# Performance work log

Measured on AMD Instinct MI355X. Metric: run time of the kernel, lower is better.

The kernel has to match this reference:

```python
import jax, jax.numpy as jnp
import numpy as np

LEAK_RATE = 0.9
SPECTRAL_RADIUS = 0.95
DENSITY = 0.1
RES_SCALE = 1.0
IN_SCALE = 0.1
H = 1024   # reservoir_size
CH = 4     # channel_size
D = 64     # input_size
B = 16
T = 1024


def setup_inputs() -> dict:
    key = jax.random.key(0)
    kx, kw, ki, km = jax.random.split(key, 4)
    x = jax.random.normal(kx, (B, CH, T, D), dtype=jnp.float32)
    # reservoir weights: uniform(-scale, scale), sparsified by density mask,
    # then rescaled so largest singular value == spectral_radius
    W = np.asarray(jax.random.uniform(kw, (H, H), minval=-RES_SCALE, maxval=RES_SCALE))
    mask = np.asarray(jax.random.uniform(km, (H, H)) < DENSITY, dtype=np.float32)
    W = W * mask
    rho = float(np.linalg.svd(W, compute_uv=False).max())
    if rho > 0:
        W = W * (SPECTRAL_RADIUS / rho)
    W_res = jnp.asarray(W, dtype=jnp.float32)
    W_in = jax.random.uniform(ki, (H, D * CH), minval=-IN_SCALE, maxval=IN_SCALE, dtype=jnp.float32)
    return {"x": x, "W_in": W_in, "W_res": W_res}


def reference(x, W_in, W_res):
    Bsz, ch, Tlen, Din = x.shape
    # u_t = x[:,:,t,:].reshape(B, ch*D); precompute all input projections at once
    u = jnp.transpose(x, (2, 0, 1, 3)).reshape(Tlen, Bsz, ch * Din)   # [T, B, ch*D]
    inp = jnp.einsum('tbf,hf->tbh', u, W_in)                           # [T, B, H]

    def step(state, inp_t):
        # state: [B, ch, H]; inp_t: [B, H] broadcast over channels (unsqueeze(1))
        state_update = jnp.einsum('bch,hk->bck', state, W_res)
        new_state = LEAK_RATE * jnp.tanh(inp_t[:, None, :] + state_update) \
                    + (1.0 - LEAK_RATE) * state
        return new_state, new_state

    init = jnp.zeros((Bsz, ch, W_res.shape[0]), dtype=x.dtype)
    _, states = jax.lax.scan(step, init, inp)          # [T, B, ch, H]
    return jnp.transpose(states, (1, 2, 0, 3))          # [B, ch, T, H]
```

## Files before the change

kernel.cpp:

```cpp
#include <hip/hip_runtime.h>
#include <stdint.h>


#define H_  1024
#define T_  1024
#define B_  16
#define CH_ 4
#define D_  64
#define F_  256

__global__ __launch_bounds__(256) void inp_gemm(const float* __restrict__ x,
                                                const float* __restrict__ W_in,
                                                float* __restrict__ out)
{
    __shared__ float U[64 * 68];
    __shared__ float Wt[64 * 66];
    const int k0 = blockIdx.x * 64;
    const int t0 = blockIdx.y * 64;
    const int b  = blockIdx.z;
    const int tid = threadIdx.x;
    const int ty = tid >> 4, tx = tid & 15;

    float4 acc[4];
    acc[0] = float4{0.f,0.f,0.f,0.f}; acc[1] = acc[0]; acc[2] = acc[0]; acc[3] = acc[0];

    for (int fc = 0; fc < 4; ++fc) {
        {
            const int t_l = tid >> 2, fs = tid & 3;
            const float* src = x + ((size_t)(b * CH_ + fc) * T_ + (t0 + t_l)) * D_ + fs * 16;
            float* dst = &U[t_l * 68 + fs * 16];
            #pragma unroll
            for (int q = 0; q < 4; ++q)
                ((float4*)dst)[q] = ((const float4*)src)[q];
        }
        {
            const int k_l = tid >> 2, fs = tid & 3;
            const float* src = W_in + (size_t)(k0 + k_l) * F_ + fc * 64 + fs * 16;
            float4 v[4];
            #pragma unroll
            for (int q = 0; q < 4; ++q) v[q] = ((const float4*)src)[q];
            #pragma unroll
            for (int q = 0; q < 4; ++q) {
                Wt[(fs*16 + q*4 + 0) * 66 + k_l] = v[q].x;
                Wt[(fs*16 + q*4 + 1) * 66 + k_l] = v[q].y;
                Wt[(fs*16 + q*4 + 2) * 66 + k_l] = v[q].z;
                Wt[(fs*16 + q*4 + 3) * 66 + k_l] = v[q].w;
            }
        }
        __syncthreads();
        #pragma unroll 4
        for (int f4 = 0; f4 < 16; ++f4) {
            float4 a[4], bk[4];
            #pragma unroll
            for (int r = 0; r < 4; ++r)  a[r]  = *(const float4*)&U[(ty*4 + r) * 68 + f4*4];
            #pragma unroll
            for (int kk = 0; kk < 4; ++kk) bk[kk] = *(const float4*)&Wt[(f4*4 + kk) * 66 + tx*4];
            #pragma unroll
            for (int r = 0; r < 4; ++r) {
                const float4 av = a[r];
                acc[r].x = fmaf(av.x, bk[0].x, acc[r].x); acc[r].y = fmaf(av.x, bk[0].y, acc[r].y);
                acc[r].z = fmaf(av.x, bk[0].z, acc[r].z); acc[r].w = fmaf(av.x, bk[0].w, acc[r].w);
                acc[r].x = fmaf(av.y, bk[1].x, acc[r].x); acc[r].y = fmaf(av.y, bk[1].y, acc[r].y);
                acc[r].z = fmaf(av.y, bk[1].z, acc[r].z); acc[r].w = fmaf(av.y, bk[1].w, acc[r].w);
                acc[r].x = fmaf(av.z, bk[2].x, acc[r].x); acc[r].y = fmaf(av.z, bk[2].y, acc[r].y);
                acc[r].z = fmaf(av.z, bk[2].z, acc[r].z); acc[r].w = fmaf(av.z, bk[2].w, acc[r].w);
                acc[r].x = fmaf(av.w, bk[3].x, acc[r].x); acc[r].y = fmaf(av.w, bk[3].y, acc[r].y);
                acc[r].z = fmaf(av.w, bk[3].z, acc[r].z); acc[r].w = fmaf(av.w, bk[3].w, acc[r].w);
            }
        }
        __syncthreads();
    }
    #pragma unroll
    for (int r = 0; r < 4; ++r) {
        float* dst = out + ((size_t)(b * CH_) * T_ + (t0 + ty*4 + r)) * H_ + k0 + tx*4;
        *(float4*)dst = acc[r];
    }
}

#define LOAD32_SC0(v, a0, a1)                                                     \
    asm volatile(                                                                 \
        "global_load_dwordx2 %0, %32, off sc0\n\t"                                \
        "global_load_dwordx2 %1, %32, off offset:256 sc0\n\t"                     \
        "global_load_dwordx2 %2, %32, off offset:512 sc0\n\t"                     \
        "global_load_dwordx2 %3, %32, off offset:768 sc0\n\t"                     \
        "global_load_dwordx2 %4, %32, off offset:1024 sc0\n\t"                    \
        "global_load_dwordx2 %5, %32, off offset:1280 sc0\n\t"                    \
        "global_load_dwordx2 %6, %32, off offset:1536 sc0\n\t"                    \
        "global_load_dwordx2 %7, %32, off offset:1792 sc0\n\t"                    \
        "global_load_dwordx2 %8, %32, off offset:2048 sc0\n\t"                    \
        "global_load_dwordx2 %9, %32, off offset:2304 sc0\n\t"                    \
        "global_load_dwordx2 %10, %32, off offset:2560 sc0\n\t"                   \
        "global_load_dwordx2 %11, %32, off offset:2816 sc0\n\t"                   \
        "global_load_dwordx2 %12, %32, off offset:3072 sc0\n\t"                   \
        "global_load_dwordx2 %13, %32, off offset:3328 sc0\n\t"                   \
        "global_load_dwordx2 %14, %32, off offset:3584 sc0\n\t"                   \
        "global_load_dwordx2 %15, %32, off offset:3840 sc0\n\t"                   \
        "global_load_dwordx2 %16, %33, off sc0\n\t"                               \
        "global_load_dwordx2 %17, %33, off offset:256 sc0\n\t"                    \
        "global_load_dwordx2 %18, %33, off offset:512 sc0\n\t"                    \
        "global_load_dwordx2 %19, %33, off offset:768 sc0\n\t"                    \
        "global_load_dwordx2 %20, %33, off offset:1024 sc0\n\t"                   \
        "global_load_dwordx2 %21, %33, off offset:1280 sc0\n\t"                   \
        "global_load_dwordx2 %22, %33, off offset:1536 sc0\n\t"                   \
        "global_load_dwordx2 %23, %33, off offset:1792 sc0\n\t"                   \
        "global_load_dwordx2 %24, %33, off offset:2048 sc0\n\t"                   \
        "global_load_dwordx2 %25, %33, off offset:2304 sc0\n\t"                   \
        "global_load_dwordx2 %26, %33, off offset:2560 sc0\n\t"                   \
        "global_load_dwordx2 %27, %33, off offset:2816 sc0\n\t"                   \
        "global_load_dwordx2 %28, %33, off offset:3072 sc0\n\t"                   \
        "global_load_dwordx2 %29, %33, off offset:3328 sc0\n\t"                   \
        "global_load_dwordx2 %30, %33, off offset:3584 sc0\n\t"                   \
        "global_load_dwordx2 %31, %33, off offset:3840 sc0\n\t"                   \
        "s_waitcnt vmcnt(0)"                                                      \
        : "=&v"(v[0]),  "=&v"(v[1]),  "=&v"(v[2]),  "=&v"(v[3]),                  \
          "=&v"(v[4]),  "=&v"(v[5]),  "=&v"(v[6]),  "=&v"(v[7]),                  \
          "=&v"(v[8]),  "=&v"(v[9]),  "=&v"(v[10]), "=&v"(v[11]),                 \
          "=&v"(v[12]), "=&v"(v[13]), "=&v"(v[14]), "=&v"(v[15]),                 \
          "=&v"(v[16]), "=&v"(v[17]), "=&v"(v[18]), "=&v"(v[19]),                 \
          "=&v"(v[20]), "=&v"(v[21]), "=&v"(v[22]), "=&v"(v[23]),                 \
          "=&v"(v[24]), "=&v"(v[25]), "=&v"(v[26]), "=&v"(v[27]),                 \
          "=&v"(v[28]), "=&v"(v[29]), "=&v"(v[30]), "=&v"(v[31])                  \
        : "v"(a0), "v"(a1)                                                        \
        : "memory")

__global__ __launch_bounds__(256, 1) void esn_recur(const float* __restrict__ Wres,
                                                    float* __restrict__ out,
                                                    unsigned long long* __restrict__ hbuf)
{
    __shared__ float smem[17664];
    const int bx  = blockIdx.x;
    const int grp = bx & 7;
    const int j   = bx >> 3;
    const int C0  = j * 32;
    const int tid = threadIdx.x;
    const int kr  = tid >> 3;
    const int cg  = tid & 7;
    const int es   = tid >> 5;
    const int ecol = tid & 31;
    const int bc   = grp * 8 + es;
    const size_t seqBase = (size_t)bc * (T_ * H_);
    const size_t inpBase = (size_t)(bc & ~3) * (T_ * H_);

    float4 w4[32];
    #pragma unroll
    for (int kk = 0; kk < 32; ++kk)
        w4[kk] = *(const float4*)&Wres[(size_t)(kr * 32 + kk) * H_ + C0 + cg * 4];

    for (int idx = tid; idx < 17664; idx += 256) smem[idx] = 0.f;
    __syncthreads();

    int use_fast = 1;
    unsigned long long  pend_pv   = 0;
    unsigned long long* pend_addr = nullptr;

    for (int t = 0; t < T_; ++t) {
        float inp_v;
        if (t > 0) {
            unsigned long long v[32];
            const unsigned long long* src =
                hbuf + ((size_t)(((t - 1) & 1) * 64 + bc)) * H_ + ecol;
            const unsigned long long a0 = (unsigned long long)src;
            const unsigned long long a1 = a0 + 4096;
            const unsigned int want = (unsigned int)t;
            unsigned int bad = 1u;
            if (use_fast) {
                int spins = 0;
                for (;;) {
                    LOAD32_SC0(v, a0, a1);
                    bad = 0u;
                    #pragma unroll
                    for (int q = 0; q < 32; ++q)
                        bad |= ((unsigned int)(v[q] >> 32)) ^ want;
                    if (!bad) break;
                    if (++spins >= 64) break;
                    __builtin_amdgcn_s_sleep(1);
                }
                if (bad) use_fast = 0;
            }
            if (bad) {
                int guard = 0;
                for (;;) {
                    #pragma unroll
                    for (int q = 0; q < 32; ++q)
                        v[q] = __hip_atomic_load(src + q * 32,
                                                 __ATOMIC_RELAXED, __HIP_MEMORY_SCOPE_AGENT);
                    unsigned int b2 = 0u;
                    #pragma unroll
                    for (int q = 0; q < 32; ++q)
                        b2 |= ((unsigned int)(v[q] >> 32)) ^ want;
                    if (!b2 || ++guard > (1 << 16)) break;
                    __builtin_amdgcn_s_sleep(2);
                }
            }
            inp_v = out[inpBase + (size_t)t * H_ + C0 + ecol];
            float* dst = &smem[es * 1152 + ecol];
            #pragma unroll
            for (int q = 0; q < 32; ++q)
                dst[q * 36] = __uint_as_float((unsigned int)(v[q] & 0xffffffffu));
        } else {
            inp_v = out[inpBase + C0 + ecol];
        }
        __syncthreads();

        if (t > 0)
            __hip_atomic_store(pend_addr, pend_pv,
                               __ATOMIC_RELAXED, __HIP_MEMORY_SCOPE_AGENT);

        float4 acc4[8];
        #pragma unroll
        for (int s = 0; s < 8; ++s) acc4[s] = float4{0.f,0.f,0.f,0.f};
        const int hbase = kr * 36;
        #pragma unroll
        for (int c8 = 0; c8 < 8; ++c8) {
            const float4 wv0 = w4[c8*4+0], wv1 = w4[c8*4+1], wv2 = w4[c8*4+2], wv3 = w4[c8*4+3];
            #pragma unroll
            for (int s = 0; s < 8; ++s) {
                const float4 hv = *(const float4*)&smem[s * 1152 + hbase + c8 * 4];
                float4 a = acc4[s];
                a.x = fmaf(hv.x, wv0.x, a.x); a.y = fmaf(hv.x, wv0.y, a.y);
                a.z = fmaf(hv.x, wv0.z, a.z); a.w = fmaf(hv.x, wv0.w, a.w);
                a.x = fmaf(hv.y, wv1.x, a.x); a.y = fmaf(hv.y, wv1.y, a.y);
                a.z = fmaf(hv.y, wv1.z, a.z); a.w = fmaf(hv.y, wv1.w, a.w);
                a.x = fmaf(hv.z, wv2.x, a.x); a.y = fmaf(hv.z, wv2.y, a.y);
                a.z = fmaf(hv.z, wv2.z, a.z); a.w = fmaf(hv.z, wv2.w, a.w);
                a.x = fmaf(hv.w, wv3.x, a.x); a.y = fmaf(hv.w, wv3.y, a.y);
                a.z = fmaf(hv.w, wv3.z, a.z); a.w = fmaf(hv.w, wv3.w, a.w);
                acc4[s] = a;
            }
        }
        #pragma unroll
        for (int s = 0; s < 8; ++s) {
            float* pp = &smem[9216 + s * 1056 + kr * 33 + cg * 4];
            pp[0] = acc4[s].x; pp[1] = acc4[s].y; pp[2] = acc4[s].z; pp[3] = acc4[s].w;
        }
        __syncthreads();

        float s0 = 0.f, s1 = 0.f, s2 = 0.f, s3 = 0.f;
        #pragma unroll
        for (int k2 = 0; k2 < 32; k2 += 4) {
            s0 += smem[9216 + es * 1056 + (k2+0) * 33 + ecol];
            s1 += smem[9216 + es * 1056 + (k2+1) * 33 + ecol];
            s2 += smem[9216 + es * 1056 + (k2+2) * 33 + ecol];
            s3 += smem[9216 + es * 1056 + (k2+3) * 33 + ecol];
        }
        const float sum   = (s0 + s1) + (s2 + s3);
        const float h_old = smem[es * 1152 + j * 36 + ecol];
        const float pre = inp_v + sum;
        const float nv  = 0.9f * tanhf(pre) + 0.1f * h_old;

        unsigned long long* paddr = hbuf + ((size_t)((t & 1) * 64 + bc)) * H_ + C0 + ecol;
        const unsigned long long pv =
            ((unsigned long long)(unsigned int)(t + 1) << 32)
            | (unsigned long long)__float_as_uint(nv);
        asm volatile("global_store_dwordx2 %0, %1, off sc0"
                     :: "v"((unsigned long long)paddr), "v"(pv) : "memory");
        out[seqBase + (size_t)t * H_ + C0 + ecol] = nv;
        pend_pv = pv; pend_addr = paddr;

        __syncthreads();
    }
}

extern "C" void kernel_launch(void* const* d_in, const int* in_sizes, int n_in,
                              void* d_out, int out_size, void* d_ws, size_t ws_size,
                              hipStream_t stream) {
    const float* x    = (const float*)d_in[0];
    const float* W_in = (const float*)d_in[1];
    const float* Wres = (const float*)d_in[2];
    float* out = (float*)d_out;
    unsigned long long* hbuf = (unsigned long long*)d_ws;

    hipMemsetAsync(hbuf, 0, 2ull * 64 * 1024 * sizeof(unsigned long long), stream);
    inp_gemm<<<dim3(16, 16, 16), 256, 0, stream>>>(x, W_in, out);
    esn_recur<<<dim3(256), 256, 0, stream>>>(Wres, out, hbuf);
}
```

Measured before the change: 4.834 ms.

## Double-buffer hidden state in LDS, drop trailing barrier, use packed FMA

```diff
diff --git a/kernel.cpp b/kernel.cpp
--- a/kernel.cpp
+++ b/kernel.cpp
@@ -8,6 +8,8 @@
 #define CH_ 4
 #define D_  64
 #define F_  256
+
+typedef float f32x2 __attribute__((ext_vector_type(2)));
 
 __global__ __launch_bounds__(256) void inp_gemm(const float* __restrict__ x,
                                                 const float* __restrict__ W_in,
@@ -127,7 +129,7 @@
                                                     float* __restrict__ out,
                                                     unsigned long long* __restrict__ hbuf)
 {
-    __shared__ float smem[17664];
+    __shared__ float smem[26880];
     const int bx  = blockIdx.x;
     const int grp = bx & 7;
     const int j   = bx >> 3;
@@ -146,7 +148,7 @@
     for (int kk = 0; kk < 32; ++kk)
         w4[kk] = *(const float4*)&Wres[(size_t)(kr * 32 + kk) * H_ + C0 + cg * 4];
 
-    for (int idx = tid; idx < 17664; idx += 256) smem[idx] = 0.f;
+    for (int idx = tid; idx < 18432; idx += 256) smem[idx] = 0.f;
     __syncthreads();
 
     int use_fast = 1;
@@ -154,7 +156,9 @@
     unsigned long long* pend_addr = nullptr;
 
     for (int t = 0; t < T_; ++t) {
-        float inp_v;
+        const float inp_v = out[inpBase + (size_t)t * H_ + C0 + ecol];
+        float* const hreg = smem + (t & 1) * 9216;
+
         if (t > 0) {
             unsigned long long v[32];
             const unsigned long long* src =
@@ -192,13 +196,10 @@
                     __builtin_amdgcn_s_sleep(2);
                 }
             }
-            inp_v = out[inpBase + (size_t)t * H_ + C0 + ecol];
-            float* dst = &smem[es * 1152 + ecol];
+            float* dst = &hreg[es * 1152 + ecol];
             #pragma unroll
             for (int q = 0; q < 32; ++q)
                 dst[q * 36] = __uint_as_float((unsigned int)(v[q] & 0xffffffffu));
-        } else {
-            inp_v = out[inpBase + C0 + ecol];
         }
         __syncthreads();
 
@@ -206,45 +207,49 @@
             __hip_atomic_store(pend_addr, pend_pv,
                                __ATOMIC_RELAXED, __HIP_MEMORY_SCOPE_AGENT);
 
-        float4 acc4[8];
-        #pragma unroll
-        for (int s = 0; s < 8; ++s) acc4[s] = float4{0.f,0.f,0.f,0.f};
+        f32x2 acc[8][2];
+        #pragma unroll
+        for (int s = 0; s < 8; ++s) { acc[s][0] = (f32x2){0.f,0.f}; acc[s][1] = (f32x2){0.f,0.f}; }
         const int hbase = kr * 36;
         #pragma unroll
         for (int c8 = 0; c8 < 8; ++c8) {
             const float4 wv0 = w4[c8*4+0], wv1 = w4[c8*4+1], wv2 = w4[c8*4+2], wv3 = w4[c8*4+3];
+            const f32x2 w00 = {wv0.x, wv0.y}, w01 = {wv0.z, wv0.w};
+            const f32x2 w10 = {wv1.x, wv1.y}, w11 = {wv1.z, wv1.w};
+            const f32x2 w20 = {wv2.x, wv2.y}, w21 = {wv2.z, wv2.w};
+            const f32x2 w30 = {wv3.x, wv3.y}, w31 = {wv3.z, wv3.w};
             #pragma unroll
             for (int s = 0; s < 8; ++s) {
-                const float4 hv = *(const float4*)&smem[s * 1152 + hbase + c8 * 4];
-                float4 a = acc4[s];
-                a.x = fmaf(hv.x, wv0.x, a.x); a.y = fmaf(hv.x, wv0.y, a.y);
-                a.z = fmaf(hv.x, wv0.z, a.z); a.w = fmaf(hv.x, wv0.w, a.w);
-                a.x = fmaf(hv.y, wv1.x, a.x); a.y = fmaf(hv.y, wv1.y, a.y);
-                a.z = fmaf(hv.y, wv1.z, a.z); a.w = fmaf(hv.y, wv1.w, a.w);
-                a.x = fmaf(hv.z, wv2.x, a.x); a.y = fmaf(hv.z, wv2.y, a.y);
-                a.z = fmaf(hv.z, wv2.z, a.z); a.w = fmaf(hv.z, wv2.w, a.w);
-                a.x = fmaf(hv.w, wv3.x, a.x); a.y = fmaf(hv.w, wv3.y, a.y);
-                a.z = fmaf(hv.w, wv3.z, a.z); a.w = fmaf(hv.w, wv3.w, a.w);
-                acc4[s] = a;
+                const float4 hv = *(const float4*)&hreg[s * 1152 + hbase + c8 * 4];
+                const f32x2 hx = {hv.x, hv.x}, hy = {hv.y, hv.y};
+                const f32x2 hz = {hv.z, hv.z}, hw = {hv.w, hv.w};
+                acc[s][0] = __builtin_elementwise_fma(hx, w00, acc[s][0]);
+                acc[s][1] = __builtin_elementwise_fma(hx, w01, acc[s][1]);
+                acc[s][0] = __builtin_elementwise_fma(hy, w10, acc[s][0]);
+                acc[s][1] = __builtin_elementwise_fma(hy, w11, acc[s][1]);
+                acc[s][0] = __builtin_elementwise_fma(hz, w20, acc[s][0]);
+                acc[s][1] = __builtin_elementwise_fma(hz, w21, acc[s][1]);
+                acc[s][0] = __builtin_elementwise_fma(hw, w30, acc[s][0]);
+                acc[s][1] = __builtin_elementwise_fma(hw, w31, acc[s][1]);
             }
         }
         #pragma unroll
         for (int s = 0; s < 8; ++s) {
-            float* pp = &smem[9216 + s * 1056 + kr * 33 + cg * 4];
-            pp[0] = acc4[s].x; pp[1] = acc4[s].y; pp[2] = acc4[s].z; pp[3] = acc4[s].w;
+            float* pp = &smem[18432 + s * 1056 + kr * 33 + cg * 4];
+            pp[0] = acc[s][0].x; pp[1] = acc[s][0].y; pp[2] = acc[s][1].x; pp[3] = acc[s][1].y;
         }
         __syncthreads();
 
         float s0 = 0.f, s1 = 0.f, s2 = 0.f, s3 = 0.f;
         #pragma unroll
         for (int k2 = 0; k2 < 32; k2 += 4) {
-            s0 += smem[9216 + es * 1056 + (k2+0) * 33 + ecol];
-            s1 += smem[9216 + es * 1056 + (k2+1) * 33 + ecol];
-            s2 += smem[9216 + es * 1056 + (k2+2) * 33 + ecol];
-            s3 += smem[9216 + es * 1056 + (k2+3) * 33 + ecol];
+            s0 += smem[18432 + es * 1056 + (k2+0) * 33 + ecol];
+            s1 += smem[18432 + es * 1056 + (k2+1) * 33 + ecol];
+            s2 += smem[18432 + es * 1056 + (k2+2) * 33 + ecol];
+            s3 += smem[18432 + es * 1056 + (k2+3) * 33 + ecol];
         }
         const float sum   = (s0 + s1) + (s2 + s3);
-        const float h_old = smem[es * 1152 + j * 36 + ecol];
+        const float h_old = hreg[es * 1152 + j * 36 + ecol];
         const float pre = inp_v + sum;
         const float nv  = 0.9f * tanhf(pre) + 0.1f * h_old;
 
@@ -255,9 +260,9 @@
         asm volatile("global_store_dwordx2 %0, %1, off sc0"
                      :: "v"((unsigned long long)paddr), "v"(pv) : "memory");
         out[seqBase + (size_t)t * H_ + C0 + ecol] = nv;
+        if (!use_fast)
+            __hip_atomic_store(paddr, pv, __ATOMIC_RELAXED, __HIP_MEMORY_SCOPE_AGENT);
         pend_pv = pv; pend_addr = paddr;
-
-        __syncthreads();
     }
 }
 
```

Measured after the change: 5.777 ms. +19.5%, slower.
